# Performance work log

Measured on AMD Instinct MI355X. Metric: run time of the kernel, lower is better.

Reference implementation:

```python
import jax, jax.numpy as jnp
import numpy as np

N_NODES = 100000
N_EDGES = 1600000
IN_DIM = 64
HID = 128
N_GRAPHS = 64
N_CLASSES = 2
EPS = 1e-5


def setup_inputs() -> dict:
    key = jax.random.key(0)
    ks = jax.random.split(key, 8)
    x = jax.random.normal(ks[0], (N_NODES, IN_DIM), dtype=jnp.float32)
    edge_index = jax.random.randint(ks[1], (2, N_EDGES), 0, N_NODES, dtype=jnp.int64)
    batch = jnp.sort(jax.random.randint(ks[2], (N_NODES,), 0, N_GRAPHS, dtype=jnp.int64))
    W1 = jax.random.normal(ks[3], (IN_DIM, HID), dtype=jnp.float32) / np.sqrt(IN_DIM)
    b1 = jnp.zeros((HID,), jnp.float32)
    W2 = jax.random.normal(ks[4], (HID, HID), dtype=jnp.float32) / np.sqrt(HID)
    b2 = jnp.zeros((HID,), jnp.float32)
    gamma = jnp.ones((HID,), jnp.float32)
    beta = jnp.zeros((HID,), jnp.float32)
    fcW = jax.random.normal(ks[5], (HID, N_CLASSES), dtype=jnp.float32) / np.sqrt(HID)
    fcb = jnp.zeros((N_CLASSES,), jnp.float32)
    return {"x": x, "edge_index": edge_index, "batch": batch, "W1": W1, "b1": b1,
            "W2": W2, "b2": b2, "gamma": gamma, "beta": beta, "fcW": fcW, "fcb": fcb}


def reference(x, edge_index, batch, W1, b1, W2, b2, gamma, beta, fcW, fcb):
    n = x.shape[0]
    loop = jnp.arange(n)
    # GCNConv adds self-loops and uses symmetric normalization D^-1/2 (A+I) D^-1/2
    src = jnp.concatenate([edge_index[0], loop])
    dst = jnp.concatenate([edge_index[1], loop])
    deg = jax.ops.segment_sum(jnp.ones_like(dst, dtype=x.dtype), dst, num_segments=n)
    dis = jax.lax.rsqrt(deg)  # deg >= 1 thanks to self-loops
    enorm = dis[src] * dis[dst]  # [E+N]

    def gcn(h, W, b):
        h = h @ W                                   # transform first (PyG order)
        msg = h[src] * enorm[:, None]               # gather + scale
        return jax.ops.segment_sum(msg, dst, num_segments=n) + b  # scatter-add

    cnt = jnp.maximum(jax.ops.segment_sum(jnp.ones((n,), x.dtype), batch,
                                          num_segments=N_GRAPHS), 1.0)[:, None]

    def inst_norm(h):
        # per-graph, per-channel normalization over nodes (affine=False)
        mean = jax.ops.segment_sum(h, batch, num_segments=N_GRAPHS) / cnt
        var = jax.ops.segment_sum(h * h, batch, num_segments=N_GRAPHS) / cnt - mean * mean
        return (h - mean[batch]) * jax.lax.rsqrt(var[batch] + EPS)

    h = jax.nn.relu(inst_norm(gcn(x, W1, b1)))   # dropout = identity (eval)
    h = jax.nn.relu(inst_norm(gcn(h, W2, b2)))
    pooled = jax.ops.segment_sum(h, batch, num_segments=N_GRAPHS) / cnt  # global mean pool
    # BatchNorm1d over the graph dimension (batch statistics, affine)
    m = jnp.mean(pooled, axis=0)
    v = jnp.mean((pooled - m) ** 2, axis=0)
    z = (pooled - m) * jax.lax.rsqrt(v + EPS) * gamma + beta
    return z @ fcW + fcb
```

## Files before the change

### kernel.cpp

```cpp
#include <hip/hip_runtime.h>
#include <hip/hip_bf16.h>


#define HID 128
#define NGRAPH 64
#define EPSN 1e-5f
#define BSHIFT 8
#define NBMAX 512

typedef unsigned int uint;
typedef unsigned short ushort;
typedef __attribute__((ext_vector_type(8))) short short8;
typedef __attribute__((ext_vector_type(4))) float f32x4;

static __device__ __forceinline__ ushort f2bf(float f) {
  uint x = __float_as_uint(f);
  return (ushort)((x + 0x7FFFu + ((x >> 16) & 1u)) >> 16);
}
static __device__ __forceinline__ float bf_lo(uint u) { return __uint_as_float(u << 16); }
static __device__ __forceinline__ float bf_hi(uint u) {
  return __uint_as_float(u & 0xFFFF0000u);
}

__global__ __launch_bounds__(256) void graph_starts(const int* __restrict__ batch,
                                                    int* __restrict__ gstart, int N) {
  int i = blockIdx.x * 256 + threadIdx.x;
  if (i >= N) return;
  int g = batch[i];
  if (i == 0) {
    for (int q = 0; q <= g; ++q) gstart[q] = 0;
  } else {
    int gp = batch[i - 1];
    if (g != gp)
      for (int q = gp + 1; q <= g; ++q) gstart[q] = i;
  }
  if (i == N - 1)
    for (int q = g + 1; q <= NGRAPH; ++q) gstart[q] = N;
}

__global__ __launch_bounds__(64) void cnt_from_starts(const int* __restrict__ gstart,
                                                      float* __restrict__ cnt) {
  int g = threadIdx.x;
  if (g < NGRAPH) cnt[g] = (float)(gstart[g + 1] - gstart[g]);
}

__global__ __launch_bounds__(256) void init_cursor(int* __restrict__ gcursor, int NB, int cap) {
  int i = blockIdx.x * 256 + threadIdx.x;
  if (i < NB) gcursor[i] = i * cap;
}

__global__ __launch_bounds__(256) void bin_edges(const int* __restrict__ src,
                                                 const int* __restrict__ dst,
                                                 int* __restrict__ gcursor,
                                                 uint* __restrict__ records, int E, int NB,
                                                 int cap) {
  __shared__ int h[NBMAX];
  __shared__ int base[NBMAX];
  for (int i = threadIdx.x; i < NB; i += 256) h[i] = 0;
  __syncthreads();
  int e0 = blockIdx.x * 4096;
  int d[16], s[16];
#pragma unroll
  for (int k = 0; k < 16; ++k) {
    int e = e0 + k * 256 + threadIdx.x;
    if (e < E) {
      d[k] = dst[e];
      s[k] = src[e];
      atomicAdd(&h[d[k] >> BSHIFT], 1);
    }
  }
  __syncthreads();
  for (int i = threadIdx.x; i < NB; i += 256) {
    int c = h[i];
    if (c) base[i] = atomicAdd(&gcursor[i], c);
  }
  __syncthreads();
  for (int i = threadIdx.x; i < NB; i += 256) h[i] = 0;
  __syncthreads();
#pragma unroll
  for (int k = 0; k < 16; ++k) {
    int e = e0 + k * 256 + threadIdx.x;
    if (e < E) {
      int b = d[k] >> BSHIFT;
      int lp = atomicAdd(&h[b], 1);
      records[base[b] + lp] = ((uint)s[k] << 8) | (uint)(d[k] & 255);
    }
  }
}

__global__ __launch_bounds__(256) void build_csr(const uint* __restrict__ records,
                                                 const int* __restrict__ gcursor,
                                                 int* __restrict__ row_beg,
                                                 int* __restrict__ row_end,
                                                 float* __restrict__ dis,
                                                 int* __restrict__ esrc, int N, int cap) {
  const int b = blockIdx.x;
  const int node0 = b << BSHIFT;
  const int nn = min(256, N - node0);
  const int beg = b * cap;
  const int cnt = gcursor[b] - beg;
  const int t = threadIdx.x;
  __shared__ int lc[256], sc[256], lcur[256];
  lc[t] = 0;
  __syncthreads();
  for (int i = t; i < cnt; i += 256) atomicAdd(&lc[records[beg + i] & 255u], 1);
  __syncthreads();
  int myc = lc[t];
  sc[t] = myc;
  __syncthreads();
  for (int off = 1; off < 256; off <<= 1) {
    int add = (t >= off) ? sc[t - off] : 0;
    __syncthreads();
    sc[t] += add;
    __syncthreads();
  }
  int excl = sc[t] - myc;
  if (t < nn) {
    row_beg[node0 + t] = beg + excl;
    row_end[node0 + t] = beg + excl + myc;
    dis[node0 + t] = rsqrtf((float)myc + 1.0f);
  }
  lcur[t] = excl;
  __syncthreads();
  for (int i = t; i < cnt; i += 256) {
    uint r = records[beg + i];
    int p = atomicAdd(&lcur[r & 255u], 1);
    esrc[beg + p] = (int)(r >> 8);
  }
}

__global__ __launch_bounds__(256) void xscale_bf16(const float* __restrict__ X,
                                                   const float* __restrict__ dis,
                                                   ushort* __restrict__ XS, int n4) {
  int i4 = blockIdx.x * 256 + threadIdx.x;
  if (i4 >= n4) return;
  int n = i4 >> 4;
  float dn = dis[n];
  float4 v = ((const float4*)X)[i4];
  ushort4 u;
  u.x = f2bf(v.x * dn);
  u.y = f2bf(v.y * dn);
  u.z = f2bf(v.z * dn);
  u.w = f2bf(v.w * dn);
  ((ushort4*)XS)[i4] = u;
}

template <int K>
__global__ __launch_bounds__(256) void wt_bf16(const float* __restrict__ W,
                                               ushort* __restrict__ Wt) {
  int i = blockIdx.x * 256 + threadIdx.x;
  if (i >= 128 * K) return;
  int c = i / K;
  int k = i - c * K;
  Wt[i] = f2bf(W[(size_t)k * HID + c]);
}

__global__ __launch_bounds__(256) void aggregate64(const ushort* __restrict__ XS,
                                                   const int* __restrict__ row_beg,
                                                   const int* __restrict__ row_end,
                                                   const int* __restrict__ esrc,
                                                   const float* __restrict__ dis,
                                                   ushort* __restrict__ out, int N) {
  int wid = (int)((blockIdx.x * 256 + threadIdx.x) >> 6);
  if (wid >= N) return;
  const int lane = threadIdx.x & 63;
  const float dn = dis[wid];
  const int beg = row_beg[wid];
  const int end = row_end[wid];
  const ushort* Xl = XS + lane;
  float a0 = 0.f, a1 = 0.f, a2 = 0.f, a3 = 0.f;
  int e = beg;
  for (; e + 7 < end; e += 8) {
    int s0 = esrc[e], s1 = esrc[e + 1], s2 = esrc[e + 2], s3 = esrc[e + 3];
    int s4 = esrc[e + 4], s5 = esrc[e + 5], s6 = esrc[e + 6], s7 = esrc[e + 7];
    ushort v0 = Xl[(size_t)s0 * 64];
    ushort v1 = Xl[(size_t)s1 * 64];
    ushort v2 = Xl[(size_t)s2 * 64];
    ushort v3 = Xl[(size_t)s3 * 64];
    ushort v4 = Xl[(size_t)s4 * 64];
    ushort v5 = Xl[(size_t)s5 * 64];
    ushort v6 = Xl[(size_t)s6 * 64];
    ushort v7 = Xl[(size_t)s7 * 64];
    a0 += __uint_as_float((uint)v0 << 16) + __uint_as_float((uint)v1 << 16);
    a1 += __uint_as_float((uint)v2 << 16) + __uint_as_float((uint)v3 << 16);
    a2 += __uint_as_float((uint)v4 << 16) + __uint_as_float((uint)v5 << 16);
    a3 += __uint_as_float((uint)v6 << 16) + __uint_as_float((uint)v7 << 16);
  }
  for (; e + 1 < end; e += 2) {
    ushort v0 = Xl[(size_t)esrc[e] * 64];
    ushort v1 = Xl[(size_t)esrc[e + 1] * 64];
    a0 += __uint_as_float((uint)v0 << 16);
    a1 += __uint_as_float((uint)v1 << 16);
  }
  if (e < end) a0 += __uint_as_float((uint)Xl[(size_t)esrc[e] * 64] << 16);
  a0 += a1 + a2 + a3 + __uint_as_float((uint)Xl[(size_t)wid * 64] << 16);
  out[(size_t)wid * 64 + lane] = f2bf(a0 * dn);
}

__global__ __launch_bounds__(256) void aggregate128(const ushort* __restrict__ H,
                                                    const int* __restrict__ row_beg,
                                                    const int* __restrict__ row_end,
                                                    const int* __restrict__ esrc,
                                                    const float* __restrict__ dis,
                                                    const float* __restrict__ bias,
                                                    ushort* __restrict__ outz, int N) {
  int wid = (int)((blockIdx.x * 256 + threadIdx.x) >> 6);
  if (wid >= N) return;
  const int lane = threadIdx.x & 63;
  const float dn = dis[wid];
  const int beg = row_beg[wid];
  const int end = row_end[wid];
  const uint* Hl = (const uint*)H + lane;
  float a0 = 0.f, a1 = 0.f, b0 = 0.f, b1 = 0.f;
  float c0 = 0.f, c1 = 0.f, d0 = 0.f, d1 = 0.f;
  int e = beg;
  for (; e + 7 < end; e += 8) {
    int s0 = esrc[e], s1 = esrc[e + 1], s2 = esrc[e + 2], s3 = esrc[e + 3];
    int s4 = esrc[e + 4], s5 = esrc[e + 5], s6 = esrc[e + 6], s7 = esrc[e + 7];
    uint u0 = Hl[(size_t)s0 * 64];
    uint u1 = Hl[(size_t)s1 * 64];
    uint u2 = Hl[(size_t)s2 * 64];
    uint u3 = Hl[(size_t)s3 * 64];
    uint u4 = Hl[(size_t)s4 * 64];
    uint u5 = Hl[(size_t)s5 * 64];
    uint u6 = Hl[(size_t)s6 * 64];
    uint u7 = Hl[(size_t)s7 * 64];
    a0 += bf_lo(u0) + bf_lo(u1);
    a1 += bf_hi(u0) + bf_hi(u1);
    b0 += bf_lo(u2) + bf_lo(u3);
    b1 += bf_hi(u2) + bf_hi(u3);
    c0 += bf_lo(u4) + bf_lo(u5);
    c1 += bf_hi(u4) + bf_hi(u5);
    d0 += bf_lo(u6) + bf_lo(u7);
    d1 += bf_hi(u6) + bf_hi(u7);
  }
  for (; e + 1 < end; e += 2) {
    uint u0 = Hl[(size_t)esrc[e] * 64];
    uint u1 = Hl[(size_t)esrc[e + 1] * 64];
    a0 += bf_lo(u0);
    a1 += bf_hi(u0);
    b0 += bf_lo(u1);
    b1 += bf_hi(u1);
  }
  if (e < end) {
    uint u0 = Hl[(size_t)esrc[e] * 64];
    a0 += bf_lo(u0);
    a1 += bf_hi(u0);
  }
  uint us = Hl[(size_t)wid * 64];
  a0 += b0 + c0 + d0 + bf_lo(us);
  a1 += b1 + c1 + d1 + bf_hi(us);
  float2 b = ((const float2*)bias)[lane];
  float r0 = a0 * dn + b.x;
  float r1 = a1 * dn + b.y;
  ((uint*)outz)[(size_t)wid * 64 + lane] = (uint)f2bf(r0) | ((uint)f2bf(r1) << 16);
}

template <int K, bool FUSE_NORM, bool DIS_SCALE, bool HAS_BIAS>
__global__ __launch_bounds__(256) void gemm_mfma(const ushort* __restrict__ X,
                                                 const ushort* __restrict__ Wt,
                                                 const float* __restrict__ bias,
                                                 const int* __restrict__ batch,
                                                 const float* __restrict__ mean,
                                                 const float* __restrict__ inv,
                                                 const float* __restrict__ disv,
                                                 ushort* __restrict__ Y, int N) {
  const int t = threadIdx.x;
  const int w = t >> 6;
  const int l = t & 63;
  const int lr = l & 15;
  const int lk = l >> 4;
  const int row0 = blockIdx.x * 64 + w * 16;
  const int arow = min(row0 + lr, N - 1);
  int g = 0;
  if (FUSE_NORM) g = batch[arow];
  f32x4 acc[8];
#pragma unroll
  for (int i = 0; i < 8; ++i) acc[i] = (f32x4){0.f, 0.f, 0.f, 0.f};
#pragma unroll
  for (int k0 = 0; k0 < K; k0 += 32) {
    const int kbase = k0 + lk * 8;
    short8 a = *(const short8*)(X + (size_t)arow * K + kbase);
    if (FUSE_NORM) {
      const float* mp = mean + g * HID + kbase;
      const float* ip = inv + g * HID + kbase;
      short8 an;
#pragma unroll
      for (int j = 0; j < 8; ++j) {
        float f = __uint_as_float((uint)(ushort)a[j] << 16);
        f = fmaxf((f - mp[j]) * ip[j], 0.f);
        an[j] = (short)f2bf(f);
      }
      a = an;
    }
#pragma unroll
    for (int nf = 0; nf < 8; ++nf) {
      short8 b = *(const short8*)(Wt + (size_t)(nf * 16 + lr) * K + kbase);
      acc[nf] = __builtin_amdgcn_mfma_f32_16x16x32_bf16(a, b, acc[nf], 0, 0, 0);
    }
  }
#pragma unroll
  for (int r = 0; r < 4; ++r) {
    int grow = row0 + lk * 4 + r;
    if (grow < N) {
      float ds = DIS_SCALE ? disv[grow] : 1.f;
#pragma unroll
      for (int nf = 0; nf < 8; ++nf) {
        int col = nf * 16 + lr;
        float v = acc[nf][r];
        if (HAS_BIAS) v += bias[col];
        v *= ds;
        Y[(size_t)grow * HID + col] = f2bf(v);
      }
    }
  }
}

__global__ __launch_bounds__(256) void stats_pass(const ushort* __restrict__ G,
                                                  const int* __restrict__ batch,
                                                  float* __restrict__ gsum,
                                                  float* __restrict__ gsq, int N) {
  const int c = threadIdx.x & 127;
  const int half = threadIdx.x >> 7;
  const int n0 = blockIdx.x * 64 + half * 32;
  const int n1 = min(n0 + 32, N);
  float s = 0.f, sq = 0.f;
  int cur = -1;
  for (int n = n0; n < n1; ++n) {
    int g = batch[n];
    if (g != cur) {
      if (cur >= 0) {
        atomicAdd(&gsum[cur * HID + c], s);
        atomicAdd(&gsq[cur * HID + c], sq);
      }
      cur = g;
      s = 0.f;
      sq = 0.f;
    }
    float val = __uint_as_float((uint)G[(size_t)n * HID + c] << 16);
    s += val;
    sq += val * val;
  }
  if (cur >= 0) {
    atomicAdd(&gsum[cur * HID + c], s);
    atomicAdd(&gsq[cur * HID + c], sq);
  }
}

__global__ __launch_bounds__(256) void finalize_stats(const float* __restrict__ gsum,
                                                      const float* __restrict__ gsq,
                                                      const float* __restrict__ cnt,
                                                      float* __restrict__ mean,
                                                      float* __restrict__ inv) {
  int i = blockIdx.x * 256 + threadIdx.x;
  if (i >= NGRAPH * HID) return;
  int g = i >> 7;
  float c = fmaxf(cnt[g], 1.f);
  float m = gsum[i] / c;
  float v = gsq[i] / c - m * m;
  mean[i] = m;
  inv[i] = rsqrtf(v + EPSN);
}

__global__ __launch_bounds__(256) void norm_relu_pool(const ushort* __restrict__ G,
                                                      const int* __restrict__ batch,
                                                      const float* __restrict__ mean,
                                                      const float* __restrict__ inv,
                                                      float* __restrict__ pooled, int N) {
  const int c = threadIdx.x & 127;
  const int half = threadIdx.x >> 7;
  const int n0 = blockIdx.x * 64 + half * 32;
  const int n1 = min(n0 + 32, N);
  float s = 0.f;
  int cur = -1;
  for (int n = n0; n < n1; ++n) {
    int g = batch[n];
    if (g != cur) {
      if (cur >= 0) atomicAdd(&pooled[cur * HID + c], s);
      cur = g;
      s = 0.f;
    }
    float val = __uint_as_float((uint)G[(size_t)n * HID + c] << 16);
    float v = (val - mean[g * HID + c]) * inv[g * HID + c];
    s += fmaxf(v, 0.f);
  }
  if (cur >= 0) atomicAdd(&pooled[cur * HID + c], s);
}

__global__ __launch_bounds__(256) void final_head(const float* __restrict__ pooled_sum,
                                                  const float* __restrict__ cnt,
                                                  const float* __restrict__ gamma,
                                                  const float* __restrict__ beta,
                                                  const float* __restrict__ fcW,
                                                  const float* __restrict__ fcb,
                                                  float* __restrict__ out) {
  __shared__ float P[NGRAPH][HID];
  __shared__ float zs[HID], zb[HID];
  int t = threadIdx.x;
  for (int i = t; i < NGRAPH * HID; i += 256) {
    int g = i >> 7;
    P[g][i & 127] = pooled_sum[i] / fmaxf(cnt[g], 1.f);
  }
  __syncthreads();
  if (t < HID) {
    float m = 0.f;
    for (int g = 0; g < NGRAPH; ++g) m += P[g][t];
    m *= (1.f / NGRAPH);
    float v = 0.f;
    for (int g = 0; g < NGRAPH; ++g) {
      float d = P[g][t] - m;
      v += d * d;
    }
    v *= (1.f / NGRAPH);
    float sc = rsqrtf(v + EPSN) * gamma[t];
    zs[t] = sc;
    zb[t] = beta[t] - m * sc;
  }
  __syncthreads();
  if (t < NGRAPH * 2) {
    int g = t >> 1, k = t & 1;
    float acc = fcb[k];
    for (int c = 0; c < HID; ++c) {
      float z = P[g][c] * zs[c] + zb[c];
      acc += z * fcW[c * 2 + k];
    }
    out[t] = acc;
  }
}

extern "C" void kernel_launch(void* const* d_in, const int* in_sizes, int n_in,
                              void* d_out, int out_size, void* d_ws, size_t ws_size,
                              hipStream_t stream) {
  const float* x = (const float*)d_in[0];
  const int* ei = (const int*)d_in[1];
  const int* batch = (const int*)d_in[2];
  const float* W1 = (const float*)d_in[3];
  const float* b1 = (const float*)d_in[4];
  const float* W2 = (const float*)d_in[5];
  const float* b2 = (const float*)d_in[6];
  const float* gamma = (const float*)d_in[7];
  const float* beta = (const float*)d_in[8];
  const float* fcW = (const float*)d_in[9];
  const float* fcb = (const float*)d_in[10];
  float* out = (float*)d_out;

  const int N = in_sizes[2];
  const int E = in_sizes[1] / 2;
  const int* srcp = ei;
  const int* dstp = ei + E;
  const int NB = (N + 255) >> BSHIFT;
  const int cap = 2 * (E / NB) + 256;

  float* ws = (float*)d_ws;
  size_t off = 0;
  auto alloc = [&](size_t n) {
    float* p = ws + off;
    off += (n + 127) & ~(size_t)127;
    return p;
  };
  int* row_beg = (int*)alloc(N);
  int* row_end = (int*)alloc(N);
  int* esrc = (int*)alloc((size_t)NB * cap);
  size_t recsz = ((size_t)NB * cap > (size_t)N * 32 ? (size_t)NB * cap : (size_t)N * 32);
  float* recbuf = alloc(recsz);
  float* dis = alloc(N);
  float* y1b = alloc((size_t)N * 32);
  float* h1b = alloc((size_t)N * 64);
  float* h2b = alloc((size_t)N * 64);
  float* zb_ = alloc((size_t)N * 64);
  float* w1tb = alloc(128 * 64 / 2);
  float* w2tb = alloc(128 * 128 / 2);
  int* gcursor = (int*)alloc(NBMAX);
  int* gstart = (int*)alloc(NGRAPH + 1);
  float* zero0 = ws + off;
  float* gsum1 = alloc(NGRAPH * HID);
  float* gsq1 = alloc(NGRAPH * HID);
  float* gsum2 = alloc(NGRAPH * HID);
  float* gsq2 = alloc(NGRAPH * HID);
  float* pooled = alloc(NGRAPH * HID);
  size_t zero_bytes = (size_t)((ws + off) - zero0) * sizeof(float);
  float* cnt = alloc(NGRAPH);
  float* mean1 = alloc(NGRAPH * HID);
  float* inv1 = alloc(NGRAPH * HID);
  float* mean2 = alloc(NGRAPH * HID);
  float* inv2 = alloc(NGRAPH * HID);

  uint* records = (uint*)recbuf;
  ushort* xs = (ushort*)recbuf;
  ushort* y1 = (ushort*)y1b;
  ushort* h1 = (ushort*)h1b;
  ushort* h2s = (ushort*)h2b;
  ushort* z = (ushort*)zb_;
  ushort* w1t = (ushort*)w1tb;
  ushort* w2t = (ushort*)w2tb;

  const int nblkN = (N + 255) / 256;
  const int nblkE4k = (E + 4095) / 4096;

  hipMemsetAsync(zero0, 0, zero_bytes, stream);

  wt_bf16<64><<<(128 * 64 + 255) / 256, 256, 0, stream>>>(W1, w1t);
  wt_bf16<128><<<(128 * 128 + 255) / 256, 256, 0, stream>>>(W2, w2t);

  graph_starts<<<nblkN, 256, 0, stream>>>(batch, gstart, N);
  cnt_from_starts<<<1, 64, 0, stream>>>(gstart, cnt);
  init_cursor<<<(NB + 255) / 256, 256, 0, stream>>>(gcursor, NB, cap);
  bin_edges<<<nblkE4k, 256, 0, stream>>>(srcp, dstp, gcursor, records, E, NB, cap);
  build_csr<<<NB, 256, 0, stream>>>(records, gcursor, row_beg, row_end, dis, esrc, N, cap);

  const int aggBlocks = (N + 3) / 4;
  const int gemmBlocks = (N + 63) / 64;

  xscale_bf16<<<(N * 16 + 255) / 256, 256, 0, stream>>>(x, dis, xs, N * 16);
  aggregate64<<<aggBlocks, 256, 0, stream>>>(xs, row_beg, row_end, esrc, dis, y1, N);
  gemm_mfma<64, false, false, true><<<gemmBlocks, 256, 0, stream>>>(
      y1, w1t, b1, nullptr, nullptr, nullptr, nullptr, h1, N);
  stats_pass<<<(N + 63) / 64, 256, 0, stream>>>(h1, batch, gsum1, gsq1, N);
  finalize_stats<<<(NGRAPH * HID + 255) / 256, 256, 0, stream>>>(gsum1, gsq1, cnt, mean1, inv1);

  gemm_mfma<128, true, true, false><<<gemmBlocks, 256, 0, stream>>>(
      h1, w2t, nullptr, batch, mean1, inv1, dis, h2s, N);
  aggregate128<<<aggBlocks, 256, 0, stream>>>(h2s, row_beg, row_end, esrc, dis, b2, z, N);
  stats_pass<<<(N + 63) / 64, 256, 0, stream>>>(z, batch, gsum2, gsq2, N);
  finalize_stats<<<(NGRAPH * HID + 255) / 256, 256, 0, stream>>>(gsum2, gsq2, cnt, mean2, inv2);
  norm_relu_pool<<<(N + 63) / 64, 256, 0, stream>>>(z, batch, mean2, inv2, pooled, N);

  final_head<<<1, 256, 0, stream>>>(pooled, cnt, gamma, beta, fcW, fcb, out);
}
```

Measured before the change: 307.6 us.

## Widen per-lane gathers in aggregation, vectorize stats passes, drop tiny launches

```diff
diff --git a/kernel.cpp b/kernel.cpp
--- a/kernel.cpp
+++ b/kernel.cpp
@@ -38,17 +38,6 @@
     for (int q = g + 1; q <= NGRAPH; ++q) gstart[q] = N;
 }
 
-__global__ __launch_bounds__(64) void cnt_from_starts(const int* __restrict__ gstart,
-                                                      float* __restrict__ cnt) {
-  int g = threadIdx.x;
-  if (g < NGRAPH) cnt[g] = (float)(gstart[g + 1] - gstart[g]);
-}
-
-__global__ __launch_bounds__(256) void init_cursor(int* __restrict__ gcursor, int NB, int cap) {
-  int i = blockIdx.x * 256 + threadIdx.x;
-  if (i < NB) gcursor[i] = i * cap;
-}
-
 __global__ __launch_bounds__(256) void bin_edges(const int* __restrict__ src,
                                                  const int* __restrict__ dst,
                                                  int* __restrict__ gcursor,
@@ -72,7 +61,7 @@
   __syncthreads();
   for (int i = threadIdx.x; i < NB; i += 256) {
     int c = h[i];
-    if (c) base[i] = atomicAdd(&gcursor[i], c);
+    if (c) base[i] = i * cap + atomicAdd(&gcursor[i], c);
   }
   __syncthreads();
   for (int i = threadIdx.x; i < NB; i += 256) h[i] = 0;
@@ -98,7 +87,7 @@
   const int node0 = b << BSHIFT;
   const int nn = min(256, N - node0);
   const int beg = b * cap;
-  const int cnt = gcursor[b] - beg;
+  const int cnt = gcursor[b];
   const int t = threadIdx.x;
   __shared__ int lc[256], sc[256], lcur[256];
   lc[t] = 0;
@@ -145,14 +134,21 @@
   ((ushort4*)XS)[i4] = u;
 }
 
-template <int K>
-__global__ __launch_bounds__(256) void wt_bf16(const float* __restrict__ W,
-                                               ushort* __restrict__ Wt) {
+__global__ __launch_bounds__(256) void wt_both(const float* __restrict__ W1,
+                                               const float* __restrict__ W2,
+                                               ushort* __restrict__ w1t,
+                                               ushort* __restrict__ w2t) {
   int i = blockIdx.x * 256 + threadIdx.x;
-  if (i >= 128 * K) return;
-  int c = i / K;
-  int k = i - c * K;
-  Wt[i] = f2bf(W[(size_t)k * HID + c]);
+  if (i < 128 * 64) {
+    int c = i / 64, k = i - c * 64;
+    w1t[i] = f2bf(W1[(size_t)k * HID + c]);
+  } else {
+    int i2 = i - 128 * 64;
+    if (i2 < 128 * 128) {
+      int c = i2 / 128, k = i2 - c * 128;
+      w2t[i2] = f2bf(W2[(size_t)k * HID + c]);
+    }
+  }
 }
 
 __global__ __launch_bounds__(256) void aggregate64(const ushort* __restrict__ XS,
@@ -161,40 +157,44 @@
                                                    const int* __restrict__ esrc,
                                                    const float* __restrict__ dis,
                                                    ushort* __restrict__ out, int N) {
-  int wid = (int)((blockIdx.x * 256 + threadIdx.x) >> 6);
-  if (wid >= N) return;
-  const int lane = threadIdx.x & 63;
-  const float dn = dis[wid];
-  const int beg = row_beg[wid];
-  const int end = row_end[wid];
-  const ushort* Xl = XS + lane;
-  float a0 = 0.f, a1 = 0.f, a2 = 0.f, a3 = 0.f;
-  int e = beg;
-  for (; e + 7 < end; e += 8) {
-    int s0 = esrc[e], s1 = esrc[e + 1], s2 = esrc[e + 2], s3 = esrc[e + 3];
-    int s4 = esrc[e + 4], s5 = esrc[e + 5], s6 = esrc[e + 6], s7 = esrc[e + 7];
-    ushort v0 = Xl[(size_t)s0 * 64];
-    ushort v1 = Xl[(size_t)s1 * 64];
-    ushort v2 = Xl[(size_t)s2 * 64];
-    ushort v3 = Xl[(size_t)s3 * 64];
-    ushort v4 = Xl[(size_t)s4 * 64];
-    ushort v5 = Xl[(size_t)s5 * 64];
-    ushort v6 = Xl[(size_t)s6 * 64];
-    ushort v7 = Xl[(size_t)s7 * 64];
-    a0 += __uint_as_float((uint)v0 << 16) + __uint_as_float((uint)v1 << 16);
-    a1 += __uint_as_float((uint)v2 << 16) + __uint_as_float((uint)v3 << 16);
-    a2 += __uint_as_float((uint)v4 << 16) + __uint_as_float((uint)v5 << 16);
-    a3 += __uint_as_float((uint)v6 << 16) + __uint_as_float((uint)v7 << 16);
-  }
-  for (; e + 1 < end; e += 2) {
-    ushort v0 = Xl[(size_t)esrc[e] * 64];
-    ushort v1 = Xl[(size_t)esrc[e + 1] * 64];
-    a0 += __uint_as_float((uint)v0 << 16);
-    a1 += __uint_as_float((uint)v1 << 16);
-  }
-  if (e < end) a0 += __uint_as_float((uint)Xl[(size_t)esrc[e] * 64] << 16);
-  a0 += a1 + a2 + a3 + __uint_as_float((uint)Xl[(size_t)wid * 64] << 16);
-  out[(size_t)wid * 64 + lane] = f2bf(a0 * dn);
+  int wave = (int)((blockIdx.x * 256 + threadIdx.x) >> 6);
+  const int l = threadIdx.x & 63;
+  const int n = wave * 2 + (l >> 5);
+  if (n >= N) return;
+  const int j = l & 31;
+  const float dn = dis[n];
+  const int beg = row_beg[n];
+  const int len = row_end[n] - beg;
+  const uint* Xj = (const uint*)XS + j;
+  float a0 = 0.f, a1 = 0.f, b0 = 0.f, b1 = 0.f;
+  int i = 0;
+  for (; i + 7 < len; i += 8) {
+    int s0 = esrc[beg + i], s1 = esrc[beg + i + 1];
+    int s2 = esrc[beg + i + 2], s3 = esrc[beg + i + 3];
+    int s4 = esrc[beg + i + 4], s5 = esrc[beg + i + 5];
+    int s6 = esrc[beg + i + 6], s7 = esrc[beg + i + 7];
+    uint u0 = Xj[(size_t)s0 * 32];
+    uint u1 = Xj[(size_t)s1 * 32];
+    uint u2 = Xj[(size_t)s2 * 32];
+    uint u3 = Xj[(size_t)s3 * 32];
+    uint u4 = Xj[(size_t)s4 * 32];
+    uint u5 = Xj[(size_t)s5 * 32];
+    uint u6 = Xj[(size_t)s6 * 32];
+    uint u7 = Xj[(size_t)s7 * 32];
+    a0 += bf_lo(u0) + bf_lo(u1) + bf_lo(u2) + bf_lo(u3);
+    a1 += bf_hi(u0) + bf_hi(u1) + bf_hi(u2) + bf_hi(u3);
+    b0 += bf_lo(u4) + bf_lo(u5) + bf_lo(u6) + bf_lo(u7);
+    b1 += bf_hi(u4) + bf_hi(u5) + bf_hi(u6) + bf_hi(u7);
+  }
+  for (; i < len; ++i) {
+    uint u = Xj[(size_t)esrc[beg + i] * 32];
+    a0 += bf_lo(u);
+    a1 += bf_hi(u);
+  }
+  uint us = Xj[(size_t)n * 32];
+  a0 += b0 + bf_lo(us);
+  a1 += b1 + bf_hi(us);
+  ((uint*)out)[(size_t)n * 32 + j] = (uint)f2bf(a0 * dn) | ((uint)f2bf(a1 * dn) << 16);
 }
 
 __global__ __launch_bounds__(256) void aggregate128(const ushort* __restrict__ H,
@@ -204,56 +204,57 @@
                                                     const float* __restrict__ dis,
                                                     const float* __restrict__ bias,
                                                     ushort* __restrict__ outz, int N) {
-  int wid = (int)((blockIdx.x * 256 + threadIdx.x) >> 6);
-  if (wid >= N) return;
-  const int lane = threadIdx.x & 63;
-  const float dn = dis[wid];
-  const int beg = row_beg[wid];
-  const int end = row_end[wid];
-  const uint* Hl = (const uint*)H + lane;
-  float a0 = 0.f, a1 = 0.f, b0 = 0.f, b1 = 0.f;
-  float c0 = 0.f, c1 = 0.f, d0 = 0.f, d1 = 0.f;
-  int e = beg;
-  for (; e + 7 < end; e += 8) {
-    int s0 = esrc[e], s1 = esrc[e + 1], s2 = esrc[e + 2], s3 = esrc[e + 3];
-    int s4 = esrc[e + 4], s5 = esrc[e + 5], s6 = esrc[e + 6], s7 = esrc[e + 7];
-    uint u0 = Hl[(size_t)s0 * 64];
-    uint u1 = Hl[(size_t)s1 * 64];
-    uint u2 = Hl[(size_t)s2 * 64];
-    uint u3 = Hl[(size_t)s3 * 64];
-    uint u4 = Hl[(size_t)s4 * 64];
-    uint u5 = Hl[(size_t)s5 * 64];
-    uint u6 = Hl[(size_t)s6 * 64];
-    uint u7 = Hl[(size_t)s7 * 64];
-    a0 += bf_lo(u0) + bf_lo(u1);
-    a1 += bf_hi(u0) + bf_hi(u1);
-    b0 += bf_lo(u2) + bf_lo(u3);
-    b1 += bf_hi(u2) + bf_hi(u3);
-    c0 += bf_lo(u4) + bf_lo(u5);
-    c1 += bf_hi(u4) + bf_hi(u5);
-    d0 += bf_lo(u6) + bf_lo(u7);
-    d1 += bf_hi(u6) + bf_hi(u7);
-  }
-  for (; e + 1 < end; e += 2) {
-    uint u0 = Hl[(size_t)esrc[e] * 64];
-    uint u1 = Hl[(size_t)esrc[e + 1] * 64];
-    a0 += bf_lo(u0);
-    a1 += bf_hi(u0);
-    b0 += bf_lo(u1);
-    b1 += bf_hi(u1);
-  }
-  if (e < end) {
-    uint u0 = Hl[(size_t)esrc[e] * 64];
-    a0 += bf_lo(u0);
-    a1 += bf_hi(u0);
-  }
-  uint us = Hl[(size_t)wid * 64];
-  a0 += b0 + c0 + d0 + bf_lo(us);
-  a1 += b1 + c1 + d1 + bf_hi(us);
-  float2 b = ((const float2*)bias)[lane];
-  float r0 = a0 * dn + b.x;
-  float r1 = a1 * dn + b.y;
-  ((uint*)outz)[(size_t)wid * 64 + lane] = (uint)f2bf(r0) | ((uint)f2bf(r1) << 16);
+  int wave = (int)((blockIdx.x * 256 + threadIdx.x) >> 6);
+  const int l = threadIdx.x & 63;
+  const int n = wave * 2 + (l >> 5);
+  if (n >= N) return;
+  const int j = l & 31;
+  const float dn = dis[n];
+  const int beg = row_beg[n];
+  const int len = row_end[n] - beg;
+  const uint2* Hj = (const uint2*)H + j;
+  float a0 = 0.f, a1 = 0.f, a2 = 0.f, a3 = 0.f;
+  float b0 = 0.f, b1 = 0.f, b2 = 0.f, b3 = 0.f;
+  int i = 0;
+  for (; i + 7 < len; i += 8) {
+    int s0 = esrc[beg + i], s1 = esrc[beg + i + 1];
+    int s2 = esrc[beg + i + 2], s3 = esrc[beg + i + 3];
+    int s4 = esrc[beg + i + 4], s5 = esrc[beg + i + 5];
+    int s6 = esrc[beg + i + 6], s7 = esrc[beg + i + 7];
+    uint2 u0 = Hj[(size_t)s0 * 32];
+    uint2 u1 = Hj[(size_t)s1 * 32];
+    uint2 u2 = Hj[(size_t)s2 * 32];
+    uint2 u3 = Hj[(size_t)s3 * 32];
+    uint2 u4 = Hj[(size_t)s4 * 32];
+    uint2 u5 = Hj[(size_t)s5 * 32];
+    uint2 u6 = Hj[(size_t)s6 * 32];
+    uint2 u7 = Hj[(size_t)s7 * 32];
+    a0 += bf_lo(u0.x) + bf_lo(u1.x) + bf_lo(u2.x) + bf_lo(u3.x);
+    a1 += bf_hi(u0.x) + bf_hi(u1.x) + bf_hi(u2.x) + bf_hi(u3.x);
+    a2 += bf_lo(u0.y) + bf_lo(u1.y) + bf_lo(u2.y) + bf_lo(u3.y);
+    a3 += bf_hi(u0.y) + bf_hi(u1.y) + bf_hi(u2.y) + bf_hi(u3.y);
+    b0 += bf_lo(u4.x) + bf_lo(u5.x) + bf_lo(u6.x) + bf_lo(u7.x);
+    b1 += bf_hi(u4.x) + bf_hi(u5.x) + bf_hi(u6.x) + bf_hi(u7.x);
+    b2 += bf_lo(u4.y) + bf_lo(u5.y) + bf_lo(u6.y) + bf_lo(u7.y);
+    b3 += bf_hi(u4.y) + bf_hi(u5.y) + bf_hi(u6.y) + bf_hi(u7.y);
+  }
+  for (; i < len; ++i) {
+    uint2 u = Hj[(size_t)esrc[beg + i] * 32];
+    a0 += bf_lo(u.x);
+    a1 += bf_hi(u.x);
+    a2 += bf_lo(u.y);
+    a3 += bf_hi(u.y);
+  }
+  uint2 us = Hj[(size_t)n * 32];
+  a0 += b0 + bf_lo(us.x);
+  a1 += b1 + bf_hi(us.x);
+  a2 += b2 + bf_lo(us.y);
+  a3 += b3 + bf_hi(us.y);
+  float4 bv = ((const float4*)bias)[j];
+  uint2 o;
+  o.x = (uint)f2bf(a0 * dn + bv.x) | ((uint)f2bf(a1 * dn + bv.y) << 16);
+  o.y = (uint)f2bf(a2 * dn + bv.z) | ((uint)f2bf(a3 * dn + bv.w) << 16);
+  ((uint2*)outz)[(size_t)n * 32 + j] = o;
 }
 
 template <int K, bool FUSE_NORM, bool DIS_SCALE, bool HAS_BIAS>
@@ -320,42 +321,49 @@
                                                   const int* __restrict__ batch,
                                                   float* __restrict__ gsum,
                                                   float* __restrict__ gsq, int N) {
-  const int c = threadIdx.x & 127;
-  const int half = threadIdx.x >> 7;
-  const int n0 = blockIdx.x * 64 + half * 32;
-  const int n1 = min(n0 + 32, N);
-  float s = 0.f, sq = 0.f;
+  const int c2 = threadIdx.x & 63;
+  const int sub = threadIdx.x >> 6;
+  const int n0 = blockIdx.x * 64 + sub * 16;
+  const int n1 = min(n0 + 16, N);
+  const uint* Gj = (const uint*)G + c2;
+  float s0 = 0.f, s1 = 0.f, q0 = 0.f, q1 = 0.f;
   int cur = -1;
   for (int n = n0; n < n1; ++n) {
     int g = batch[n];
     if (g != cur) {
       if (cur >= 0) {
-        atomicAdd(&gsum[cur * HID + c], s);
-        atomicAdd(&gsq[cur * HID + c], sq);
+        atomicAdd(&gsum[cur * HID + 2 * c2], s0);
+        atomicAdd(&gsum[cur * HID + 2 * c2 + 1], s1);
+        atomicAdd(&gsq[cur * HID + 2 * c2], q0);
+        atomicAdd(&gsq[cur * HID + 2 * c2 + 1], q1);
       }
       cur = g;
-      s = 0.f;
-      sq = 0.f;
-    }
-    float val = __uint_as_float((uint)G[(size_t)n * HID + c] << 16);
-    s += val;
-    sq += val * val;
+      s0 = s1 = q0 = q1 = 0.f;
+    }
+    uint u = Gj[(size_t)n * 64];
+    float v0 = bf_lo(u), v1 = bf_hi(u);
+    s0 += v0;
+    s1 += v1;
+    q0 += v0 * v0;
+    q1 += v1 * v1;
   }
   if (cur >= 0) {
-    atomicAdd(&gsum[cur * HID + c], s);
-    atomicAdd(&gsq[cur * HID + c], sq);
+    atomicAdd(&gsum[cur * HID + 2 * c2], s0);
+    atomicAdd(&gsum[cur * HID + 2 * c2 + 1], s1);
+    atomicAdd(&gsq[cur * HID + 2 * c2], q0);
+    atomicAdd(&gsq[cur * HID + 2 * c2 + 1], q1);
   }
 }
 
 __global__ __launch_bounds__(256) void finalize_stats(const float* __restrict__ gsum,
                                                       const float* __restrict__ gsq,
-                                                      const float* __restrict__ cnt,
+                                                      const int* __restrict__ gstart,
                                                       float* __restrict__ mean,
                                                       float* __restrict__ inv) {
   int i = blockIdx.x * 256 + threadIdx.x;
   if (i >= NGRAPH * HID) return;
   int g = i >> 7;
-  float c = fmaxf(cnt[g], 1.f);
+  float c = fmaxf((float)(gstart[g + 1] - gstart[g]), 1.f);
   float m = gsum[i] / c;
   float v = gsq[i] / c - m * m;
   mean[i] = m;
@@ -367,28 +375,38 @@
                                                       const float* __restrict__ mean,
                                                       const float* __restrict__ inv,
                                                       float* __restrict__ pooled, int N) {
-  const int c = threadIdx.x & 127;
-  const int half = threadIdx.x >> 7;
-  const int n0 = blockIdx.x * 64 + half * 32;
-  const int n1 = min(n0 + 32, N);
-  float s = 0.f;
+  const int c2 = threadIdx.x & 63;
+  const int sub = threadIdx.x >> 6;
+  const int n0 = blockIdx.x * 64 + sub * 16;
+  const int n1 = min(n0 + 16, N);
+  const uint* Gj = (const uint*)G + c2;
+  float p0 = 0.f, p1 = 0.f;
   int cur = -1;
+  float2 mv = {0.f, 0.f}, iv = {0.f, 0.f};
   for (int n = n0; n < n1; ++n) {
     int g = batch[n];
     if (g != cur) {
-      if (cur >= 0) atomicAdd(&pooled[cur * HID + c], s);
+      if (cur >= 0) {
+        atomicAdd(&pooled[cur * HID + 2 * c2], p0);
+        atomicAdd(&pooled[cur * HID + 2 * c2 + 1], p1);
+      }
       cur = g;
-      s = 0.f;
-    }
-    float val = __uint_as_float((uint)G[(size_t)n * HID + c] << 16);
-    float v = (val - mean[g * HID + c]) * inv[g * HID + c];
-    s += fmaxf(v, 0.f);
-  }
-  if (cur >= 0) atomicAdd(&pooled[cur * HID + c], s);
+      p0 = p1 = 0.f;
+      mv = ((const float2*)mean)[g * 64 + c2];
+      iv = ((const float2*)inv)[g * 64 + c2];
+    }
+    uint u = Gj[(size_t)n * 64];
+    p0 += fmaxf((bf_lo(u) - mv.x) * iv.x, 0.f);
+    p1 += fmaxf((bf_hi(u) - mv.y) * iv.y, 0.f);
+  }
+  if (cur >= 0) {
+    atomicAdd(&pooled[cur * HID + 2 * c2], p0);
+    atomicAdd(&pooled[cur * HID + 2 * c2 + 1], p1);
+  }
 }
 
 __global__ __launch_bounds__(256) void final_head(const float* __restrict__ pooled_sum,
-                                                  const float* __restrict__ cnt,
+                                                  const int* __restrict__ gstart,
                                                   const float* __restrict__ gamma,
                                                   const float* __restrict__ beta,
                                                   const float* __restrict__ fcW,
@@ -399,7 +417,8 @@
   int t = threadIdx.x;
   for (int i = t; i < NGRAPH * HID; i += 256) {
     int g = i >> 7;
-    P[g][i & 127] = pooled_sum[i] / fmaxf(cnt[g], 1.f);
+    float c = fmaxf((float)(gstart[g + 1] - gstart[g]), 1.f);
+    P[g][i & 127] = pooled_sum[i] / c;
   }
   __syncthreads();
   if (t < HID) {
@@ -470,16 +489,15 @@
   float* zb_ = alloc((size_t)N * 64);
   float* w1tb = alloc(128 * 64 / 2);
   float* w2tb = alloc(128 * 128 / 2);
-  int* gcursor = (int*)alloc(NBMAX);
   int* gstart = (int*)alloc(NGRAPH + 1);
   float* zero0 = ws + off;
+  int* gcursor = (int*)alloc(NBMAX);
   float* gsum1 = alloc(NGRAPH * HID);
   float* gsq1 = alloc(NGRAPH * HID);
   float* gsum2 = alloc(NGRAPH * HID);
   float* gsq2 = alloc(NGRAPH * HID);
   float* pooled = alloc(NGRAPH * HID);
   size_t zero_bytes = (size_t)((ws + off) - zero0) * sizeof(float);
-  float* cnt = alloc(NGRAPH);
   float* mean1 = alloc(NGRAPH * HID);
   float* inv1 = alloc(NGRAPH * HID);
   float* mean2 = alloc(NGRAPH * HID);
@@ -499,31 +517,28 @@
 
   hipMemsetAsync(zero0, 0, zero_bytes, stream);
 
-  wt_bf16<64><<<(128 * 64 + 255) / 256, 256, 0, stream>>>(W1, w1t);
-  wt_bf16<128><<<(128 * 128 + 255) / 256, 256, 0, stream>>>(W2, w2t);
-
+  wt_both<<<(128 * 64 + 128 * 128 + 255) / 256, 256, 0, stream>>>(W1, W2, w1t, w2t);
   graph_starts<<<nblkN, 256, 0, stream>>>(batch, gstart, N);
-  cnt_from_starts<<<1, 64, 0, stream>>>(gstart, cnt);
-  init_cursor<<<(NB + 255) / 256, 256, 0, stream>>>(gcursor, NB, cap);
   bin_edges<<<nblkE4k, 256, 0, stream>>>(srcp, dstp, gcursor, records, E, NB, cap);
   build_csr<<<NB, 256, 0, stream>>>(records, gcursor, row_beg, row_end, dis, esrc, N, cap);
 
-  const int aggBlocks = (N + 3) / 4;
+  const int aggBlocks = ((N + 1) / 2 + 3) / 4;
   const int gemmBlocks = (N + 63) / 64;
+  const int nrmBlocks = (N + 63) / 64;
 
   xscale_bf16<<<(N * 16 + 255) / 256, 256, 0, stream>>>(x, dis, xs, N * 16);
   aggregate64<<<aggBlocks, 256, 0, stream>>>(xs, row_beg, row_end, esrc, dis, y1, N);
   gemm_mfma<64, false, false, true><<<gemmBlocks, 256, 0, stream>>>(
       y1, w1t, b1, nullptr, nullptr, nullptr, nullptr, h1, N);
-  stats_pass<<<(N + 63) / 64, 256, 0, stream>>>(h1, batch, gsum1, gsq1, N);
-  finalize_stats<<<(NGRAPH * HID + 255) / 256, 256, 0, stream>>>(gsum1, gsq1, cnt, mean1, inv1);
+  stats_pass<<<nrmBlocks, 256, 0, stream>>>(h1, batch, gsum1, gsq1, N);
+  finalize_stats<<<(NGRAPH * HID + 255) / 256, 256, 0, stream>>>(gsum1, gsq1, gstart, mean1, inv1);
 
   gemm_mfma<128, true, true, false><<<gemmBlocks, 256, 0, stream>>>(
       h1, w2t, nullptr, batch, mean1, inv1, dis, h2s, N);
   aggregate128<<<aggBlocks, 256, 0, stream>>>(h2s, row_beg, row_end, esrc, dis, b2, z, N);
-  stats_pass<<<(N + 63) / 64, 256, 0, stream>>>(z, batch, gsum2, gsq2, N);
-  finalize_stats<<<(NGRAPH * HID + 255) / 256, 256, 0, stream>>>(gsum2, gsq2, cnt, mean2, inv2);
-  norm_relu_pool<<<(N + 63) / 64, 256, 0, stream>>>(z, batch, mean2, inv2, pooled, N);
-
-  final_head<<<1, 256, 0, stream>>>(pooled, cnt, gamma, beta, fcW, fcb, out);
-}
+  stats_pass<<<nrmBlocks, 256, 0, stream>>>(z, batch, gsum2, gsq2, N);
+  finalize_stats<<<(NGRAPH * HID + 255) / 256, 256, 0, stream>>>(gsum2, gsq2, gstart, mean2, inv2);
+  norm_relu_pool<<<nrmBlocks, 256, 0, stream>>>(z, batch, mean2, inv2, pooled, N);
+
+  final_head<<<1, 256, 0, stream>>>(pooled, gstart, gamma, beta, fcW, fcb, out);
+}
```

Result: no change. 302.6 us (-1.6%).
